# Kernel tuning notes

Measured on AMD Instinct MI355X. Metric: run time of the kernel, lower is better.

## Reference

```python
import jax, jax.numpy as jnp
import numpy as np

FEAT_DIM = 2048
HID = 256
N = 1024
NUM_CLASSES = 16
BN_EPS = 1e-5


def _batchnorm(x, gamma, beta):
    # training-mode BatchNorm1d: per-batch mean, biased variance
    m = x.mean(axis=0)
    v = x.var(axis=0)
    return gamma * (x - m) / jnp.sqrt(v + BN_EPS) + beta


def setup_inputs() -> dict:
    key = jax.random.key(0)
    ks = jax.random.split(key, 12)
    s1 = 1.0 / np.sqrt(FEAT_DIM)
    s2 = 1.0 / np.sqrt(HID)
    s3 = 1.0 / np.sqrt(2 * HID)
    return {
        "features": jax.random.normal(ks[0], (N, FEAT_DIM), dtype=jnp.float32),
        "labels": jax.random.randint(ks[1], (N,), 0, NUM_CLASSES, dtype=jnp.int32),
        # semantic disentangler
        "W1": jax.random.normal(ks[2], (FEAT_DIM, HID), dtype=jnp.float32) * s1,
        "b1": jnp.zeros((HID,), jnp.float32),
        "g1": jnp.ones((HID,), jnp.float32),
        "bt1": jnp.zeros((HID,), jnp.float32),
        "W2": jax.random.normal(ks[3], (HID, HID), dtype=jnp.float32) * s2,
        "b2": jnp.zeros((HID,), jnp.float32),
        "g2": jnp.ones((HID,), jnp.float32),
        "bt2": jnp.zeros((HID,), jnp.float32),
        # edge network: Linear(2H -> H), Linear(H -> 1)
        "We1": jax.random.normal(ks[4], (2 * HID, HID), dtype=jnp.float32) * s3,
        "bwe1": jnp.zeros((HID,), jnp.float32),
        "We2": jax.random.normal(ks[5], (HID, 1), dtype=jnp.float32) * s2,
        "bwe2": jnp.zeros((1,), jnp.float32),
    }


def reference(features, labels, W1, b1, g1, bt1, W2, b2, g2, bt2,
              We1, bwe1, We2, bwe2):
    # semantic disentangler: (Linear -> BN -> ReLU) x2
    h = jax.nn.relu(_batchnorm(features @ W1 + b1, g1, bt1))
    di = jax.nn.relu(_batchnorm(h @ W2 + b2, g2, bt2))  # [N, H]

    # EdgeNetwork all-pairs: Linear on concat([f_i, f_j]) splits into two GEMMs
    hi = di @ We1[:HID]   # [N, H] contribution of node i (first half of concat)
    hj = di @ We1[HID:]   # [N, H] contribution of node j (second half)
    pair = jax.nn.relu(hi[:, None, :] + hj[None, :, :] + bwe1)  # [N, N, H]
    logits = pair @ We2[:, 0] + bwe2[0]                          # [N, N]
    same_label = labels[:, None] == labels[None, :]
    off_diag = ~jnp.eye(N, dtype=bool)
    edge_weights = jnp.where(same_label & off_diag,
                             jax.nn.sigmoid(logits), 0.0)        # [N, N]

    # update_node_features: f_i + sum_j w_ij f_j / sum_j w_ij (if wsum > 0)
    weighted_sum = edge_weights @ di                 # [N, H] (w_ii == 0)
    wsum = edge_weights.sum(axis=1, keepdims=True)   # [N, 1]
    denom = jnp.where(wsum > 0, wsum, 1.0)
    updated = di + jnp.where(wsum > 0, weighted_sum / denom, 0.0)
    return updated
```

## Files before the change

kernel.cpp:

```cpp
#include <hip/hip_runtime.h>
#include <math.h>

#define N_PTS 1024
#define HID   256
#define FEAT  2048

typedef short bf16x8 __attribute__((ext_vector_type(8)));
typedef float f32x4  __attribute__((ext_vector_type(4)));

__device__ inline ushort f2bf(float f) {
    union { float f; unsigned u; } v; v.f = f;
    unsigned r = v.u + 0x7fff + ((v.u >> 16) & 1);
    return (ushort)(r >> 16);
}

__global__ __launch_bounds__(256) void prep(
    const float* __restrict__ features, const float* __restrict__ W1,
    const float* __restrict__ W2, const float* __restrict__ We1,
    ushort* __restrict__ Af, ushort* __restrict__ W1T,
    ushort* __restrict__ W2T, ushort* __restrict__ WeT)
{
    const int tid = threadIdx.x;
    int b = blockIdx.x;
    if (b < 512) {
        #pragma unroll
        for (int q = 0; q < 2; q++) {
            const size_t g = (size_t)b * 256 + tid + (size_t)q * 131072;
            float4 v0 = ((const float4*)features)[g * 2];
            float4 v1 = ((const float4*)features)[g * 2 + 1];
            bf16x8 o;
            o[0] = (short)f2bf(v0.x); o[1] = (short)f2bf(v0.y);
            o[2] = (short)f2bf(v0.z); o[3] = (short)f2bf(v0.w);
            o[4] = (short)f2bf(v1.x); o[5] = (short)f2bf(v1.y);
            o[6] = (short)f2bf(v1.z); o[7] = (short)f2bf(v1.w);
            ((bf16x8*)Af)[g] = o;
        }
        return;
    }
    __shared__ ushort Ts[64 * 72];
    const float* src; ushort* dst; int K;
    b -= 512;
    if (b < 128)      { src = W1;  dst = W1T; K = 2048; }
    else if (b < 144) { b -= 128; src = W2;  dst = W2T; K = 256; }
    else              { b -= 144; src = We1; dst = WeT; K = 512; }
    const int k0 = (b >> 2) * 64;
    const int n0 = (b & 3) * 64;
    #pragma unroll
    for (int p = 0; p < 4; p++) {
        const int c  = p * 256 + tid;
        const int r  = c >> 4;
        const int cq = c & 15;
        float4 v = *(const float4*)&src[(size_t)(k0 + r) * 256 + n0 + cq * 4];
        Ts[(cq * 4 + 0) * 72 + r] = f2bf(v.x);
        Ts[(cq * 4 + 1) * 72 + r] = f2bf(v.y);
        Ts[(cq * 4 + 2) * 72 + r] = f2bf(v.z);
        Ts[(cq * 4 + 3) * 72 + r] = f2bf(v.w);
    }
    __syncthreads();
    #pragma unroll
    for (int p = 0; p < 2; p++) {
        const int c    = p * 256 + tid;
        const int row  = c >> 3;
        const int col8 = c & 7;
        *(bf16x8*)&dst[(size_t)(n0 + row) * K + k0 + col8 * 8] =
            *(bf16x8*)&Ts[row * 72 + col8 * 8];
    }
}

__global__ __launch_bounds__(256) void gemm1s(
    const ushort* __restrict__ A , const ushort* __restrict__ B ,
    float* __restrict__ X , float* __restrict__ statsP)
{
    __shared__ ushort As[16 * 136];
    __shared__ ushort Bs[64 * 136];
    const int tid  = threadIdx.x;
    const int lane = tid & 63;
    const int w    = tid >> 6;
    const int quad = lane >> 4, l16 = lane & 15;
    const int mBase = blockIdx.y * 16;
    const int nBase = blockIdx.x * 64;

    f32x4 acc = {};
    for (int ks = 0; ks < FEAT; ks += 128) {
        {
            const int row  = tid >> 4;
            const int col8 = tid & 15;
            *(bf16x8*)&As[row * 136 + col8 * 8] =
                *(const bf16x8*)&A[(size_t)(mBase + row) * FEAT + ks + col8 * 8];
        }
        #pragma unroll
        for (int p = 0; p < 4; p++) {
            const int c    = p * 256 + tid;
            const int row  = c >> 4;
            const int col8 = c & 15;
            *(bf16x8*)&Bs[row * 136 + col8 * 8] =
                *(const bf16x8*)&B[(size_t)(nBase + row) * FEAT + ks + col8 * 8];
        }
        __syncthreads();
        #pragma unroll
        for (int kt = 0; kt < 128; kt += 32) {
            bf16x8 af = *(bf16x8*)&As[l16 * 136 + kt + quad * 8];
            bf16x8 bf = *(bf16x8*)&Bs[(w * 16 + l16) * 136 + kt + quad * 8];
            acc = __builtin_amdgcn_mfma_f32_16x16x32_bf16(af, bf, acc, 0, 0, 0);
        }
        __syncthreads();
    }
    float sv = 0.f, qv = 0.f;
    #pragma unroll
    for (int e = 0; e < 4; e++) {
        const int gm = mBase + quad * 4 + e;
        const int gn = nBase + w * 16 + l16;
        X[(size_t)gm * HID + gn] = acc[e];
        sv += acc[e];
        qv = fmaf(acc[e], acc[e], qv);
    }
    sv += __shfl_xor(sv, 16, 64); sv += __shfl_xor(sv, 32, 64);
    qv += __shfl_xor(qv, 16, 64); qv += __shfl_xor(qv, 32, 64);
    if (quad == 0) {
        const int c = nBase + w * 16 + l16;
        statsP[blockIdx.y * 512 + c]       = sv;
        statsP[blockIdx.y * 512 + 256 + c] = qv;
    }
}

__global__ __launch_bounds__(256) void gemm2_fused(
    const float* __restrict__ A , const ushort* __restrict__ B ,
    float* __restrict__ C , const float* __restrict__ statsP,
    const float* __restrict__ g1, const float* __restrict__ bt1,
    float* __restrict__ stats2P)
{
    __shared__ ushort As[64 * 72];
    __shared__ ushort Bs[64 * 72];
    __shared__ float sscale[HID];
    __shared__ float sshift[HID];
    __shared__ float csum[64];
    __shared__ float csq[64];
    const int tid  = threadIdx.x;
    const int lane = tid & 63;
    const int wave = tid >> 6;
    const int wy = wave >> 1, wx = wave & 1;
    const int quad = lane >> 4, l16 = lane & 15;
    const int mBase = blockIdx.y * 64;
    const int nBase = blockIdx.x * 64;

    {
        float s1 = 0.f, q1 = 0.f;
        #pragma unroll 8
        for (int y = 0; y < 64; y++) {
            s1 += statsP[y * 512 + tid];
            q1 += statsP[y * 512 + 256 + tid];
        }
        float m   = s1 * (1.f / 1024.f);
        float var = fmaf(-m, m, q1 * (1.f / 1024.f));
        float rstd = rsqrtf(var + 1e-5f);
        float sc = g1[tid] * rstd;
        sscale[tid] = sc;
        sshift[tid] = fmaf(-m, sc, bt1[tid]);
    }
    if (tid < 64) { csum[tid] = 0.f; csq[tid] = 0.f; }
    __syncthreads();

    f32x4 acc[2][2] = {};
    for (int ks = 0; ks < HID; ks += 64) {
        #pragma unroll
        for (int p = 0; p < 4; p++) {
            const int c  = p * 256 + tid;
            const int r  = c >> 4;
            const int cq = c & 15;
            const int k0 = ks + cq * 4;
            float4 av = *(const float4*)&A[(size_t)(mBase + r) * HID + k0];
            float v0 = fmaxf(fmaf(sscale[k0 + 0], av.x, sshift[k0 + 0]), 0.f);
            float v1 = fmaxf(fmaf(sscale[k0 + 1], av.y, sshift[k0 + 1]), 0.f);
            float v2 = fmaxf(fmaf(sscale[k0 + 2], av.z, sshift[k0 + 2]), 0.f);
            float v3 = fmaxf(fmaf(sscale[k0 + 3], av.w, sshift[k0 + 3]), 0.f);
            ushort4 ao;
            ao.x = f2bf(v0); ao.y = f2bf(v1); ao.z = f2bf(v2); ao.w = f2bf(v3);
            *(ushort4*)&As[r * 72 + cq * 4] = ao;
        }
        #pragma unroll
        for (int p = 0; p < 2; p++) {
            const int c    = p * 256 + tid;
            const int row  = c >> 3;
            const int col8 = c & 7;
            *(bf16x8*)&Bs[row * 72 + col8 * 8] =
                *(const bf16x8*)&B[(size_t)(nBase + row) * HID + ks + col8 * 8];
        }
        __syncthreads();
        #pragma unroll
        for (int kt = 0; kt < 64; kt += 32) {
            bf16x8 af[2], bfr[2];
            #pragma unroll
            for (int mi = 0; mi < 2; mi++)
                af[mi] = *(bf16x8*)&As[(wy * 32 + mi * 16 + l16) * 72 + kt + quad * 8];
            #pragma unroll
            for (int ni = 0; ni < 2; ni++)
                bfr[ni] = *(bf16x8*)&Bs[(wx * 32 + ni * 16 + l16) * 72 + kt + quad * 8];
            #pragma unroll
            for (int mi = 0; mi < 2; mi++)
                #pragma unroll
                for (int ni = 0; ni < 2; ni++)
                    acc[mi][ni] = __builtin_amdgcn_mfma_f32_16x16x32_bf16(
                        af[mi], bfr[ni], acc[mi][ni], 0, 0, 0);
        }
        __syncthreads();
    }

    float s[2] = {0.f, 0.f}, q[2] = {0.f, 0.f};
    #pragma unroll
    for (int mi = 0; mi < 2; mi++)
        #pragma unroll
        for (int ni = 0; ni < 2; ni++)
            #pragma unroll
            for (int e = 0; e < 4; e++) {
                const int gm = mBase + wy * 32 + mi * 16 + quad * 4 + e;
                const int gn = nBase + wx * 32 + ni * 16 + l16;
                float v = acc[mi][ni][e];
                C[(size_t)gm * HID + gn] = v;
                s[ni] += v;
                q[ni] = fmaf(v, v, q[ni]);
            }
    #pragma unroll
    for (int ni = 0; ni < 2; ni++) {
        float sv = s[ni], qv = q[ni];
        sv += __shfl_xor(sv, 16, 64); sv += __shfl_xor(sv, 32, 64);
        qv += __shfl_xor(qv, 16, 64); qv += __shfl_xor(qv, 32, 64);
        if (quad == 0) {
            atomicAdd(&csum[wx * 32 + ni * 16 + l16], sv);
            atomicAdd(&csq [wx * 32 + ni * 16 + l16], qv);
        }
    }
    __syncthreads();
    if (tid < 64) {
        stats2P[blockIdx.y * 512 + nBase + tid]       = csum[tid];
        stats2P[blockIdx.y * 512 + 256 + nBase + tid] = csq[tid];
    }
}

__global__ __launch_bounds__(256) void gemm_dual_bn(
    const float* __restrict__ A , const ushort* __restrict__ WeT,
    float* __restrict__ C1 , float* __restrict__ C2 ,
    const float* __restrict__ stats2P,
    const float* __restrict__ g2, const float* __restrict__ bt2,
    float* __restrict__ di)
{
    __shared__ ushort As[64 * 72];
    __shared__ ushort Bs[64 * 72];
    __shared__ float sscale[HID];
    __shared__ float sshift[HID];
    const int tid  = threadIdx.x;
    const int lane = tid & 63;
    const int wave = tid >> 6;
    const int wy = wave >> 1, wx = wave & 1;
    const int quad = lane >> 4, l16 = lane & 15;
    const int mBase = blockIdx.y * 64;
    const int nBase = blockIdx.x * 64;
    const int half  = blockIdx.z;
    float* C = half ? C2 : C1;
    const bool writeDi = (blockIdx.x == 0) && (half == 0);

    {
        float s2 = 0.f, q2 = 0.f;
        #pragma unroll
        for (int y = 0; y < 16; y++) {
            s2 += stats2P[y * 512 + tid];
            q2 += stats2P[y * 512 + 256 + tid];
        }
        float m   = s2 * (1.f / 1024.f);
        float var = fmaf(-m, m, q2 * (1.f / 1024.f));
        float rstd = rsqrtf(var + 1e-5f);
        float sc = g2[tid] * rstd;
        sscale[tid] = sc;
        sshift[tid] = fmaf(-m, sc, bt2[tid]);
    }
    __syncthreads();

    f32x4 acc[2][2] = {};
    for (int ks = 0; ks < HID; ks += 64) {
        #pragma unroll
        for (int p = 0; p < 4; p++) {
            const int c  = p * 256 + tid;
            const int r  = c >> 4;
            const int cq = c & 15;
            const int k0 = ks + cq * 4;
            float4 av = *(const float4*)&A[(size_t)(mBase + r) * HID + k0];
            float v0 = fmaxf(fmaf(sscale[k0 + 0], av.x, sshift[k0 + 0]), 0.f);
            float v1 = fmaxf(fmaf(sscale[k0 + 1], av.y, sshift[k0 + 1]), 0.f);
            float v2 = fmaxf(fmaf(sscale[k0 + 2], av.z, sshift[k0 + 2]), 0.f);
            float v3 = fmaxf(fmaf(sscale[k0 + 3], av.w, sshift[k0 + 3]), 0.f);
            if (writeDi)
                *(float4*)&di[(size_t)(mBase + r) * HID + k0] =
                    make_float4(v0, v1, v2, v3);
            ushort4 ao;
            ao.x = f2bf(v0); ao.y = f2bf(v1); ao.z = f2bf(v2); ao.w = f2bf(v3);
            *(ushort4*)&As[r * 72 + cq * 4] = ao;
        }
        #pragma unroll
        for (int p = 0; p < 2; p++) {
            const int c    = p * 256 + tid;
            const int row  = c >> 3;
            const int col8 = c & 7;
            *(bf16x8*)&Bs[row * 72 + col8 * 8] =
                *(const bf16x8*)&WeT[(size_t)(nBase + row) * 512 + half * 256 + ks + col8 * 8];
        }
        __syncthreads();
        #pragma unroll
        for (int kt = 0; kt < 64; kt += 32) {
            bf16x8 af[2], bfr[2];
            #pragma unroll
            for (int mi = 0; mi < 2; mi++)
                af[mi] = *(bf16x8*)&As[(wy * 32 + mi * 16 + l16) * 72 + kt + quad * 8];
            #pragma unroll
            for (int ni = 0; ni < 2; ni++)
                bfr[ni] = *(bf16x8*)&Bs[(wx * 32 + ni * 16 + l16) * 72 + kt + quad * 8];
            #pragma unroll
            for (int mi = 0; mi < 2; mi++)
                #pragma unroll
                for (int ni = 0; ni < 2; ni++)
                    acc[mi][ni] = __builtin_amdgcn_mfma_f32_16x16x32_bf16(
                        af[mi], bfr[ni], acc[mi][ni], 0, 0, 0);
        }
        __syncthreads();
    }
    #pragma unroll
    for (int mi = 0; mi < 2; mi++)
        #pragma unroll
        for (int ni = 0; ni < 2; ni++)
            #pragma unroll
            for (int e = 0; e < 4; e++) {
                const int gm = mBase + wy * 32 + mi * 16 + quad * 4 + e;
                const int gn = nBase + wx * 32 + ni * 16 + l16;
                C[(size_t)gm * HID + gn] = acc[mi][ni][e];
            }
}

__global__ __launch_bounds__(256) void pair_update2(
    const float* __restrict__ di, const float* __restrict__ hi,
    const float* __restrict__ hj, const float* __restrict__ bwe1,
    const float* __restrict__ We2, const float* __restrict__ bwe2,
    const int* __restrict__ labels, float* __restrict__ out)
{
    __shared__ int   slab[N_PTS];
    __shared__ int   list[N_PTS];
    __shared__ int   cnt;
    __shared__ float sacc[16][HID];
    __shared__ float swsum[16];
    const int i   = blockIdx.x;
    const int tid = threadIdx.x;
    const int pid = tid >> 4;
    const int l16 = tid & 15;

    if (tid == 0) cnt = 0;
    for (int t = tid; t < N_PTS; t += 256) slab[t] = labels[t];
    __syncthreads();
    const int myLab = slab[i];
    for (int t = tid; t < N_PTS; t += 256)
        if (slab[t] == myLab && t != i) list[atomicAdd(&cnt, 1)] = t;
    __syncthreads();
    const int n = cnt;

    const float4* hip4 = (const float4*)(hi + (size_t)i * HID) + l16 * 4;
    const float4* bw4  = (const float4*)bwe1 + l16 * 4;
    const float4* w24  = (const float4*)We2  + l16 * 4;
    float4 hb[4], w2[4];
    #pragma unroll
    for (int s = 0; s < 4; s++) {
        float4 a = hip4[s], b = bw4[s];
        hb[s] = make_float4(a.x + b.x, a.y + b.y, a.z + b.z, a.w + b.w);
        w2[s] = w24[s];
    }
    const float b2 = bwe2[0];

    float4 acc[4] = {};
    float wloc = 0.f;
    const int rounds = (n + 15) >> 4;
    for (int r = 0; r < rounds; ++r) {
        const int idx = r * 16 + pid;
        const bool valid = idx < n;
        const int jj = valid ? list[idx] : i;
        const float4* hv4 = (const float4*)(hj + (size_t)jj * HID) + l16 * 4;
        float4 hv[4];
        #pragma unroll
        for (int s = 0; s < 4; s++) hv[s] = hv4[s];
        float p = 0.f;
        #pragma unroll
        for (int s = 0; s < 4; s++) {
            p = fmaf(fmaxf(hb[s].x + hv[s].x, 0.f), w2[s].x, p);
            p = fmaf(fmaxf(hb[s].y + hv[s].y, 0.f), w2[s].y, p);
            p = fmaf(fmaxf(hb[s].z + hv[s].z, 0.f), w2[s].z, p);
            p = fmaf(fmaxf(hb[s].w + hv[s].w, 0.f), w2[s].w, p);
        }
        p += __shfl_xor(p, 1, 64);
        p += __shfl_xor(p, 2, 64);
        p += __shfl_xor(p, 4, 64);
        p += __shfl_xor(p, 8, 64);
        const float w = valid ? 1.f / (1.f + expf(-(p + b2))) : 0.f;
        const float4* dv4 = (const float4*)(di + (size_t)jj * HID) + l16 * 4;
        #pragma unroll
        for (int s = 0; s < 4; s++) {
            float4 d = dv4[s];
            acc[s].x = fmaf(w, d.x, acc[s].x);
            acc[s].y = fmaf(w, d.y, acc[s].y);
            acc[s].z = fmaf(w, d.z, acc[s].z);
            acc[s].w = fmaf(w, d.w, acc[s].w);
        }
        if (l16 == 0) wloc += w;
    }
    #pragma unroll
    for (int s = 0; s < 4; s++)
        ((float4*)&sacc[pid][l16 * 16])[s] = acc[s];
    if (l16 == 0) swsum[pid] = wloc;
    __syncthreads();

    float at = 0.f;
    #pragma unroll
    for (int g = 0; g < 16; g++) at += sacc[g][tid];
    float wt = 0.f;
    #pragma unroll
    for (int g = 0; g < 16; g++) wt += swsum[g];
    const float dval = di[(size_t)i * HID + tid];
    out[(size_t)i * HID + tid] = dval + (wt > 0.f ? at / wt : 0.f);
}

extern "C" void kernel_launch(void* const* d_in, const int* in_sizes, int n_in,
                              void* d_out, int out_size, void* d_ws, size_t ws_size,
                              hipStream_t stream)
{
    const float* features = (const float*)d_in[0];
    const int*   labels   = (const int*)d_in[1];
    const float* W1   = (const float*)d_in[2];
    const float* g1   = (const float*)d_in[4];
    const float* bt1  = (const float*)d_in[5];
    const float* W2   = (const float*)d_in[6];
    const float* g2   = (const float*)d_in[8];
    const float* bt2  = (const float*)d_in[9];
    const float* We1  = (const float*)d_in[10];
    const float* bwe1 = (const float*)d_in[11];
    const float* We2  = (const float*)d_in[12];
    const float* bwe2 = (const float*)d_in[13];
    float* out = (float*)d_out;

    float* ws      = (float*)d_ws;
    float* x1      = ws;
    float* hi      = ws + 262144;
    float* hj      = ws + 524288;
    float* x2      = ws + 786432;
    float* di      = ws + 1048576;
    float* statsP  = ws + 1310720;
    float* stats2P = ws + 1343488;
    ushort* Af   = (ushort*)(ws + 1351680);
    ushort* W1T  = Af + 2097152;
    ushort* W2T  = W1T + 524288;
    ushort* WeT  = W2T + 65536;

    dim3 blk(256);
    prep<<<688, blk, 0, stream>>>(features, W1, W2, We1, Af, W1T, W2T, WeT);
    gemm1s<<<dim3(4, 64), blk, 0, stream>>>(Af, W1T, x1, statsP);
    gemm2_fused<<<dim3(4, 16), blk, 0, stream>>>(x1, W2T, x2, statsP,
                                                 g1, bt1, stats2P);
    gemm_dual_bn<<<dim3(4, 16, 2), blk, 0, stream>>>(x2, WeT, hi, hj,
                                                     stats2P, g2, bt2, di);
    pair_update2<<<N_PTS, blk, 0, stream>>>(di, hi, hj, bwe1, We2, bwe2,
                                            labels, out);
}
```

Before: 132.4 us.

## Fuse feature bf16 conversion into GEMM1 with split-K waves and shrink GEMM2 tiles

The separate pass that converts features to bf16 is removed. GEMM1 now reads fp32 features and converts them while loading tiles. GEMM1 switches to 32-column tiles where each wave handles its own K quarter with no block barriers, and the partial results are reduced through shared memory before the output and BN stats are written. GEMM2 uses 32x32 tiles, giving twice as many blocks in each dimension for occupancy, and the dual GEMM's stats reduction is updated to read 32 partial rows. The cost is more global fp32 reads of features, since each n-block re-reads them, plus an extra shared-memory reduction.

```diff
diff --git a/kernel.cpp b/kernel.cpp
--- a/kernel.cpp
+++ b/kernel.cpp
@@ -15,31 +15,14 @@
 }
 
 __global__ __launch_bounds__(256) void prep(
-    const float* __restrict__ features, const float* __restrict__ W1,
-    const float* __restrict__ W2, const float* __restrict__ We1,
-    ushort* __restrict__ Af, ushort* __restrict__ W1T,
+    const float* __restrict__ W1, const float* __restrict__ W2,
+    const float* __restrict__ We1, ushort* __restrict__ W1T,
     ushort* __restrict__ W2T, ushort* __restrict__ WeT)
 {
+    __shared__ ushort Ts[64 * 72];
     const int tid = threadIdx.x;
     int b = blockIdx.x;
-    if (b < 512) {
-        #pragma unroll
-        for (int q = 0; q < 2; q++) {
-            const size_t g = (size_t)b * 256 + tid + (size_t)q * 131072;
-            float4 v0 = ((const float4*)features)[g * 2];
-            float4 v1 = ((const float4*)features)[g * 2 + 1];
-            bf16x8 o;
-            o[0] = (short)f2bf(v0.x); o[1] = (short)f2bf(v0.y);
-            o[2] = (short)f2bf(v0.z); o[3] = (short)f2bf(v0.w);
-            o[4] = (short)f2bf(v1.x); o[5] = (short)f2bf(v1.y);
-            o[6] = (short)f2bf(v1.z); o[7] = (short)f2bf(v1.w);
-            ((bf16x8*)Af)[g] = o;
-        }
-        return;
-    }
-    __shared__ ushort Ts[64 * 72];
     const float* src; ushort* dst; int K;
-    b -= 512;
     if (b < 128)      { src = W1;  dst = W1T; K = 2048; }
     else if (b < 144) { b -= 128; src = W2;  dst = W2T; K = 256; }
     else              { b -= 144; src = We1; dst = WeT; K = 512; }
@@ -68,58 +51,85 @@
 }
 
 __global__ __launch_bounds__(256) void gemm1s(
-    const ushort* __restrict__ A , const ushort* __restrict__ B ,
+    const float* __restrict__ feat, const ushort* __restrict__ B ,
     float* __restrict__ X , float* __restrict__ statsP)
 {
-    __shared__ ushort As[16 * 136];
-    __shared__ ushort Bs[64 * 136];
+    __shared__ __align__(16) ushort smem[26112];
     const int tid  = threadIdx.x;
     const int lane = tid & 63;
     const int w    = tid >> 6;
     const int quad = lane >> 4, l16 = lane & 15;
     const int mBase = blockIdx.y * 16;
-    const int nBase = blockIdx.x * 64;
-
-    f32x4 acc = {};
-    for (int ks = 0; ks < FEAT; ks += 128) {
-        {
-            const int row  = tid >> 4;
-            const int col8 = tid & 15;
-            *(bf16x8*)&As[row * 136 + col8 * 8] =
-                *(const bf16x8*)&A[(size_t)(mBase + row) * FEAT + ks + col8 * 8];
-        }
+    const int nBase = blockIdx.x * 32;
+    ushort* As = smem + w * 6528;
+    ushort* Bs = As + 2176;
+
+    f32x4 acc[2] = {};
+    const int kw = w * 512;
+    for (int it = 0; it < 4; ++it) {
+        const int ks = kw + it * 128;
         #pragma unroll
         for (int p = 0; p < 4; p++) {
-            const int c    = p * 256 + tid;
+            const int c    = p * 64 + lane;
+            const int row  = c >> 4;
+            const int col8 = c & 15;
+            const float* ap = &feat[(size_t)(mBase + row) * FEAT + ks + col8 * 8];
+            float4 a0 = *(const float4*)ap;
+            float4 a1 = *(const float4*)(ap + 4);
+            bf16x8 o;
+            o[0] = (short)f2bf(a0.x); o[1] = (short)f2bf(a0.y);
+            o[2] = (short)f2bf(a0.z); o[3] = (short)f2bf(a0.w);
+            o[4] = (short)f2bf(a1.x); o[5] = (short)f2bf(a1.y);
+            o[6] = (short)f2bf(a1.z); o[7] = (short)f2bf(a1.w);
+            *(bf16x8*)&As[row * 136 + col8 * 8] = o;
+        }
+        #pragma unroll
+        for (int p = 0; p < 8; p++) {
+            const int c    = p * 64 + lane;
             const int row  = c >> 4;
             const int col8 = c & 15;
             *(bf16x8*)&Bs[row * 136 + col8 * 8] =
                 *(const bf16x8*)&B[(size_t)(nBase + row) * FEAT + ks + col8 * 8];
         }
-        __syncthreads();
         #pragma unroll
         for (int kt = 0; kt < 128; kt += 32) {
             bf16x8 af = *(bf16x8*)&As[l16 * 136 + kt + quad * 8];
-            bf16x8 bf = *(bf16x8*)&Bs[(w * 16 + l16) * 136 + kt + quad * 8];
-            acc = __builtin_amdgcn_mfma_f32_16x16x32_bf16(af, bf, acc, 0, 0, 0);
-        }
-        __syncthreads();
-    }
-    float sv = 0.f, qv = 0.f;
-    #pragma unroll
-    for (int e = 0; e < 4; e++) {
-        const int gm = mBase + quad * 4 + e;
-        const int gn = nBase + w * 16 + l16;
-        X[(size_t)gm * HID + gn] = acc[e];
-        sv += acc[e];
-        qv = fmaf(acc[e], acc[e], qv);
-    }
-    sv += __shfl_xor(sv, 16, 64); sv += __shfl_xor(sv, 32, 64);
-    qv += __shfl_xor(qv, 16, 64); qv += __shfl_xor(qv, 32, 64);
-    if (quad == 0) {
-        const int c = nBase + w * 16 + l16;
-        statsP[blockIdx.y * 512 + c]       = sv;
-        statsP[blockIdx.y * 512 + 256 + c] = qv;
+            #pragma unroll
+            for (int n = 0; n < 2; n++) {
+                bf16x8 bf = *(bf16x8*)&Bs[(n * 16 + l16) * 136 + kt + quad * 8];
+                acc[n] = __builtin_amdgcn_mfma_f32_16x16x32_bf16(af, bf, acc[n], 0, 0, 0);
+            }
+        }
+    }
+    __syncthreads();
+    float* sred = (float*)smem;
+    #pragma unroll
+    for (int n = 0; n < 2; n++)
+        #pragma unroll
+        for (int e = 0; e < 4; e++)
+            sred[(w * 16 + quad * 4 + e) * 32 + n * 16 + l16] = acc[n][e];
+    __syncthreads();
+    float* colS = sred + 2048;
+    float* colQ = colS + 256;
+    const int c  = tid & 31;
+    const int r0 = tid >> 5;
+    float v0 = 0.f, v1 = 0.f;
+    #pragma unroll
+    for (int ww = 0; ww < 4; ww++) {
+        v0 += sred[(ww * 16 + r0) * 32 + c];
+        v1 += sred[(ww * 16 + r0 + 8) * 32 + c];
+    }
+    X[(size_t)(mBase + r0) * HID + nBase + c]     = v0;
+    X[(size_t)(mBase + r0 + 8) * HID + nBase + c] = v1;
+    colS[r0 * 32 + c] = v0 + v1;
+    colQ[r0 * 32 + c] = fmaf(v0, v0, v1 * v1);
+    __syncthreads();
+    if (tid < 32) {
+        float s = 0.f, q = 0.f;
+        #pragma unroll
+        for (int r = 0; r < 8; r++) { s += colS[r * 32 + tid]; q += colQ[r * 32 + tid]; }
+        statsP[blockIdx.y * 512 + nBase + tid]       = s;
+        statsP[blockIdx.y * 512 + 256 + nBase + tid] = q;
     }
 }
 
@@ -129,19 +139,19 @@
     const float* __restrict__ g1, const float* __restrict__ bt1,
     float* __restrict__ stats2P)
 {
-    __shared__ ushort As[64 * 72];
-    __shared__ ushort Bs[64 * 72];
+    __shared__ ushort As[32 * 72];
+    __shared__ ushort Bs[32 * 72];
     __shared__ float sscale[HID];
     __shared__ float sshift[HID];
-    __shared__ float csum[64];
-    __shared__ float csq[64];
+    __shared__ float csum[2][32];
+    __shared__ float csq[2][32];
     const int tid  = threadIdx.x;
     const int lane = tid & 63;
     const int wave = tid >> 6;
     const int wy = wave >> 1, wx = wave & 1;
     const int quad = lane >> 4, l16 = lane & 15;
-    const int mBase = blockIdx.y * 64;
-    const int nBase = blockIdx.x * 64;
+    const int mBase = blockIdx.y * 32;
+    const int nBase = blockIdx.x * 32;
 
     {
         float s1 = 0.f, q1 = 0.f;
@@ -157,13 +167,12 @@
         sscale[tid] = sc;
         sshift[tid] = fmaf(-m, sc, bt1[tid]);
     }
-    if (tid < 64) { csum[tid] = 0.f; csq[tid] = 0.f; }
-    __syncthreads();
-
-    f32x4 acc[2][2] = {};
+    __syncthreads();
+
+    f32x4 acc = {};
     for (int ks = 0; ks < HID; ks += 64) {
         #pragma unroll
-        for (int p = 0; p < 4; p++) {
+        for (int p = 0; p < 2; p++) {
             const int c  = p * 256 + tid;
             const int r  = c >> 4;
             const int cq = c & 15;
@@ -177,62 +186,42 @@
             ao.x = f2bf(v0); ao.y = f2bf(v1); ao.z = f2bf(v2); ao.w = f2bf(v3);
             *(ushort4*)&As[r * 72 + cq * 4] = ao;
         }
-        #pragma unroll
-        for (int p = 0; p < 2; p++) {
-            const int c    = p * 256 + tid;
-            const int row  = c >> 3;
-            const int col8 = c & 7;
+        {
+            const int row  = tid >> 3;
+            const int col8 = tid & 7;
             *(bf16x8*)&Bs[row * 72 + col8 * 8] =
                 *(const bf16x8*)&B[(size_t)(nBase + row) * HID + ks + col8 * 8];
         }
         __syncthreads();
         #pragma unroll
         for (int kt = 0; kt < 64; kt += 32) {
-            bf16x8 af[2], bfr[2];
-            #pragma unroll
-            for (int mi = 0; mi < 2; mi++)
-                af[mi] = *(bf16x8*)&As[(wy * 32 + mi * 16 + l16) * 72 + kt + quad * 8];
-            #pragma unroll
-            for (int ni = 0; ni < 2; ni++)
-                bfr[ni] = *(bf16x8*)&Bs[(wx * 32 + ni * 16 + l16) * 72 + kt + quad * 8];
-            #pragma unroll
-            for (int mi = 0; mi < 2; mi++)
-                #pragma unroll
-                for (int ni = 0; ni < 2; ni++)
-                    acc[mi][ni] = __builtin_amdgcn_mfma_f32_16x16x32_bf16(
-                        af[mi], bfr[ni], acc[mi][ni], 0, 0, 0);
+            bf16x8 af = *(bf16x8*)&As[(wy * 16 + l16) * 72 + kt + quad * 8];
+            bf16x8 bf = *(bf16x8*)&Bs[(wx * 16 + l16) * 72 + kt + quad * 8];
+            acc = __builtin_amdgcn_mfma_f32_16x16x32_bf16(af, bf, acc, 0, 0, 0);
         }
         __syncthreads();
     }
 
-    float s[2] = {0.f, 0.f}, q[2] = {0.f, 0.f};
-    #pragma unroll
-    for (int mi = 0; mi < 2; mi++)
-        #pragma unroll
-        for (int ni = 0; ni < 2; ni++)
-            #pragma unroll
-            for (int e = 0; e < 4; e++) {
-                const int gm = mBase + wy * 32 + mi * 16 + quad * 4 + e;
-                const int gn = nBase + wx * 32 + ni * 16 + l16;
-                float v = acc[mi][ni][e];
-                C[(size_t)gm * HID + gn] = v;
-                s[ni] += v;
-                q[ni] = fmaf(v, v, q[ni]);
-            }
-    #pragma unroll
-    for (int ni = 0; ni < 2; ni++) {
-        float sv = s[ni], qv = q[ni];
-        sv += __shfl_xor(sv, 16, 64); sv += __shfl_xor(sv, 32, 64);
-        qv += __shfl_xor(qv, 16, 64); qv += __shfl_xor(qv, 32, 64);
-        if (quad == 0) {
-            atomicAdd(&csum[wx * 32 + ni * 16 + l16], sv);
-            atomicAdd(&csq [wx * 32 + ni * 16 + l16], qv);
-        }
-    }
-    __syncthreads();
-    if (tid < 64) {
-        stats2P[blockIdx.y * 512 + nBase + tid]       = csum[tid];
-        stats2P[blockIdx.y * 512 + 256 + nBase + tid] = csq[tid];
+    float s = 0.f, q = 0.f;
+    #pragma unroll
+    for (int e = 0; e < 4; e++) {
+        const int gm = mBase + wy * 16 + quad * 4 + e;
+        const int gn = nBase + wx * 16 + l16;
+        float v = acc[e];
+        C[(size_t)gm * HID + gn] = v;
+        s += v;
+        q = fmaf(v, v, q);
+    }
+    s += __shfl_xor(s, 16, 64); s += __shfl_xor(s, 32, 64);
+    q += __shfl_xor(q, 16, 64); q += __shfl_xor(q, 32, 64);
+    if (quad == 0) {
+        csum[wy][wx * 16 + l16] = s;
+        csq [wy][wx * 16 + l16] = q;
+    }
+    __syncthreads();
+    if (tid < 32) {
+        stats2P[blockIdx.y * 512 + nBase + tid]       = csum[0][tid] + csum[1][tid];
+        stats2P[blockIdx.y * 512 + 256 + nBase + tid] = csq[0][tid]  + csq[1][tid];
     }
 }
 
@@ -260,8 +249,8 @@
 
     {
         float s2 = 0.f, q2 = 0.f;
-        #pragma unroll
-        for (int y = 0; y < 16; y++) {
+        #pragma unroll 8
+        for (int y = 0; y < 32; y++) {
             s2 += stats2P[y * 512 + tid];
             q2 += stats2P[y * 512 + 256 + tid];
         }
@@ -447,15 +436,14 @@
     float* di      = ws + 1048576;
     float* statsP  = ws + 1310720;
     float* stats2P = ws + 1343488;
-    ushort* Af   = (ushort*)(ws + 1351680);
-    ushort* W1T  = Af + 2097152;
+    ushort* W1T  = (ushort*)(ws + 1359872);
     ushort* W2T  = W1T + 524288;
     ushort* WeT  = W2T + 65536;
 
     dim3 blk(256);
-    prep<<<688, blk, 0, stream>>>(features, W1, W2, We1, Af, W1T, W2T, WeT);
-    gemm1s<<<dim3(4, 64), blk, 0, stream>>>(Af, W1T, x1, statsP);
-    gemm2_fused<<<dim3(4, 16), blk, 0, stream>>>(x1, W2T, x2, statsP,
+    prep<<<176, blk, 0, stream>>>(W1, W2, We1, W1T, W2T, WeT);
+    gemm1s<<<dim3(8, 64), blk, 0, stream>>>(features, W1T, x1, statsP);
+    gemm2_fused<<<dim3(8, 32), blk, 0, stream>>>(x1, W2T, x2, statsP,
                                                  g1, bt1, stats2P);
     gemm_dual_bn<<<dim3(4, 16, 2), blk, 0, stream>>>(x2, WeT, hi, hj,
                                                      stats2P, g2, bt2, di);
```

Measured after the change: 132.3 us. Within noise of the previous version (-0.1%).
